# Kernel tuning notes

Measured on AMD Instinct MI355X. Metric: run time of the kernel, lower is better.

Reference implementation:

```python
import jax, jax.numpy as jnp
import numpy as np

P = 2        # patch size
NH = 16      # num heads
HD = 64      # head dim
OC = 4       # out channels
EPS_RMS = 1e-6
EPS_LN = 1e-5

def rmsnorm(x, w):
    return x * jax.lax.rsqrt(jnp.mean(x * x, -1, keepdims=True) + EPS_RMS) * w

def layernorm(x):  # elementwise_affine=False
    m = jnp.mean(x, -1, keepdims=True)
    v = jnp.mean((x - m) ** 2, -1, keepdims=True)
    return (x - m) * jax.lax.rsqrt(v + EPS_LN)

def rope_cache(n, hd):
    inv = 1.0 / (10000.0 ** (jnp.arange(0, hd, 2, dtype=jnp.float32) / hd))
    fr = jnp.arange(n, dtype=jnp.float32)[:, None] * inv[None, :]
    emb = jnp.concatenate([fr, fr], -1)  # [N, hd]
    return jnp.cos(emb), jnp.sin(emb)

def rotate_half(x):
    x1, x2 = jnp.split(x, 2, -1)
    return jnp.concatenate([-x2, x1], -1)

def setup_inputs() -> dict:
    key = jax.random.key(0)
    ks = iter(jax.random.split(key, 48))
    B, D, C, Sw = 8, 4, 1024, 2730
    def w(shape, s=0.02):
        return jax.random.normal(next(ks), shape, jnp.float32) * s
    return dict(
        x=jax.random.normal(next(ks), (B, 4, 32, 32), jnp.float32),
        y=jax.random.randint(next(ks), (B,), 0, 1000),
        cfg_scale=jax.random.uniform(next(ks), (B,), jnp.float32),
        patch_w=w((C, 16)), patch_b=jnp.zeros((C,), jnp.float32),
        pos_embed=w((1, 256, C)),
        class_embed=w((1001, C)),
        cfg_w1=w((C, 1)), cfg_b1=jnp.zeros((C,), jnp.float32),
        cfg_w2=w((C, C)), cfg_b2=jnp.zeros((C,), jnp.float32),
        blk_norm1_w=jnp.ones((D, C), jnp.float32), blk_norm2_w=jnp.ones((D, C), jnp.float32),
        blk_qkv_w=w((D, 3 * C, C)),
        blk_proj_w=w((D, C, C)), blk_proj_b=jnp.zeros((D, C), jnp.float32),
        blk_qn_w=jnp.ones((D, HD), jnp.float32), blk_kn_w=jnp.ones((D, HD), jnp.float32),
        blk_w1=w((D, Sw, C)), blk_w2=w((D, C, Sw)), blk_w3=w((D, Sw, C)),
        blk_ada_w=w((D, 6 * C, C)), blk_ada_b=jnp.zeros((D, 6 * C), jnp.float32),
        fin_ada_w=w((2 * C, C)), fin_ada_b=jnp.zeros((2 * C,), jnp.float32),
        fin_lin_w=w((P * P * OC, C)), fin_lin_b=jnp.zeros((P * P * OC,), jnp.float32),
    )

def reference(x, y, cfg_scale, patch_w, patch_b, pos_embed, class_embed,
              cfg_w1, cfg_b1, cfg_w2, cfg_b2,
              blk_norm1_w, blk_norm2_w, blk_qkv_w, blk_proj_w, blk_proj_b,
              blk_qn_w, blk_kn_w, blk_w1, blk_w2, blk_w3, blk_ada_w, blk_ada_b,
              fin_ada_w, fin_ada_b, fin_lin_w, fin_lin_b):
    B, Ci, Hi, Wi = x.shape
    h = Hi // P
    N = h * h
    C = patch_w.shape[0]
    scale = HD ** -0.5

    # patch embed: conv(k=2,s=2) == per-patch matmul with (Ci,p,p)-flattened weight
    patches = x.reshape(B, Ci, h, P, h, P).transpose(0, 2, 4, 1, 3, 5).reshape(B, N, Ci * P * P)
    tok = patches @ patch_w.T + patch_b + pos_embed  # [B,N,C]

    # conditioning: class embedding + cfg-scale MLP
    c = class_embed[y]
    hc = jax.nn.silu(cfg_scale[:, None] @ cfg_w1.T + cfg_b1)
    c = c + hc @ cfg_w2.T + cfg_b2  # [B,C]
    silu_c = jax.nn.silu(c)

    cos, sin = rope_cache(N, HD)  # [N,HD]
    cos = cos[None, None]
    sin = sin[None, None]

    def block(xc, p):
        n1w, n2w, qkvw, projw, projb, qnw, knw, w1, w2, w3, adaw, adab = p
        mods = silu_c @ adaw.T + adab  # [B,6C]
        sm, scm, gm, smlp, sclp, glp = jnp.split(mods, 6, -1)
        # attention branch
        xm = rmsnorm(xc, n1w) * (1 + scm[:, None]) + sm[:, None]
        qkv = (xm @ qkvw.T).reshape(B, N, 3, NH, HD).transpose(2, 0, 3, 1, 4)
        q, k, v = qkv[0], qkv[1], qkv[2]  # [B,NH,N,HD]
        q = rmsnorm(q, qnw)
        k = rmsnorm(k, knw)
        q = q * cos + rotate_half(q) * sin
        k = k * cos + rotate_half(k) * sin
        attn = jax.nn.softmax(jnp.einsum('bhqd,bhkd->bhqk', q, k) * scale, axis=-1)
        o = jnp.einsum('bhqk,bhkd->bhqd', attn, v).transpose(0, 2, 1, 3).reshape(B, N, C)
        xc = xc + gm[:, None] * (o @ projw.T + projb)
        # SwiGLU MLP branch
        xm = rmsnorm(xc, n2w) * (1 + sclp[:, None]) + smlp[:, None]
        mlp = (jax.nn.silu(xm @ w1.T) * (xm @ w3.T)) @ w2.T
        xc = xc + glp[:, None] * mlp
        return xc, None

    blk_params = (blk_norm1_w, blk_norm2_w, blk_qkv_w, blk_proj_w, blk_proj_b,
                  blk_qn_w, blk_kn_w, blk_w1, blk_w2, blk_w3, blk_ada_w, blk_ada_b)
    tok, _ = jax.lax.scan(block, tok, blk_params)

    # final layer
    shift, scl = jnp.split(silu_c @ fin_ada_w.T + fin_ada_b, 2, -1)
    out = layernorm(tok) * (1 + scl[:, None]) + shift[:, None]
    out = out @ fin_lin_w.T + fin_lin_b  # [B,N,P*P*OC]

    # unpatchify: (B,h,w,p,p,c) -> (B,c,h*p,w*p)
    out = out.reshape(B, h, h, P, P, OC).transpose(0, 5, 1, 3, 2, 4).reshape(B, OC, h * P, h * P)
    return out
```

## Files before the change

### kernel.cpp

```cpp
#include <hip/hip_runtime.h>

typedef unsigned char u8;
typedef unsigned short u16;
typedef unsigned int u32;
typedef float f32x4 __attribute__((ext_vector_type(4)));
typedef __bf16 bf16x8 __attribute__((ext_vector_type(8)));

#define DEV __device__ __forceinline__

DEV u16 f2bf(float f) {
  u32 u = __builtin_bit_cast(u32, f);
  u += 0x7fffu + ((u >> 16) & 1u);
  return (u16)(u >> 16);
}
DEV float bf2f(u16 u) { return __builtin_bit_cast(float, (u32)u << 16); }
DEV u32 f2f8(float f) {
  u32 u = __builtin_bit_cast(u32, f);
  u32 s = (u >> 31) << 7;
  float a = __builtin_fabsf(f);
  if (a >= 448.f) return s | 0x7Eu;
  if (a < 0.015625f) {
    int m = (int)(a * 512.f + 0.5f);
    return s | (u32)m;
  }
  u32 b = __builtin_bit_cast(u32, a);
  b += 0x7FFFFu + ((b >> 20) & 1u);
  u32 E = (b >> 23) - 120u;
  if (E > 15u) return s | 0x7Eu;
  return s | (E << 3) | ((b >> 20) & 7u);
}
DEV u32 pk4f8(float x, float y, float z, float w) {
  return f2f8(x) | (f2f8(y) << 8) | (f2f8(z) << 16) | (f2f8(w) << 24);
}
DEV float waveAllSum(float x) {
#pragma unroll
  for (int off = 32; off > 0; off >>= 1) x += __shfl_xor(x, off, 64);
  return x;
}
DEV float silu_f(float x) { return x / (1.f + __expf(-x)); }

DEV void gll16(const void* g, void* l) {
  __builtin_amdgcn_global_load_lds(
      (const __attribute__((address_space(1))) void*)g,
      (__attribute__((address_space(3))) void*)l, 16, 0, 0);
}

template<int BM, int BN, int EPI>
__global__ __launch_bounds__(256, (BM == 128 ? 2 : 3)) void gemm8_t(
    const u8* __restrict__ A, int lda,
    const u8* __restrict__ W, int ldw,
    int Ksteps, int nbx,
    float* __restrict__ RX, const float* __restrict__ gmods,
    const float* __restrict__ bias,
    u16* __restrict__ ob0, u16* __restrict__ ob1, u16* __restrict__ ob2,
    u8* __restrict__ h1o,
    const float* __restrict__ nw_q, const float* __restrict__ nw_k)
{
  constexpr int MI = BM / 32;
  constexpr int NJ = BN / 32;
  constexpr int LOADS = (BM + BN) / 32;
  __shared__ long As[2][BM][16];
  __shared__ long Ws[2][BN][16];
  const int tid = threadIdx.x;
  const int lane = tid & 63;
  const int wave = tid >> 6;
  const int nwg = gridDim.x;
  const int cpx = nwg >> 3;
  const int fb = blockIdx.x;
  const int idx = (fb & 7) * cpx + (fb >> 3);
  const int m0 = (idx % nbx) * BM;
  const int n0 = (idx / nbx) * BN;
  const int wm = (wave >> 1) * (BM / 2);
  const int wn = (wave & 1) * (BN / 2);
  const int rl = lane & 15;
  const int qq = lane >> 4;
  const u8* Abase = A + (size_t)m0 * lda;
  const u8* Wbase = W + (size_t)n0 * ldw;

  f32x4 acc[MI][NJ];
#pragma unroll
  for (int i = 0; i < MI; ++i)
#pragma unroll
    for (int j = 0; j < NJ; ++j) acc[i][j] = (f32x4){0.f, 0.f, 0.f, 0.f};

  auto STAGE = [&](int buf, int k0) {
#pragma unroll
    for (int c = 0; c < BM / 32; ++c) {
      const int flat = c * 256 + tid;
      const int row = flat >> 3;
      const int ch = flat & 7;
      gll16(Abase + (size_t)row * lda + k0 + ((ch ^ (row & 7)) << 4),
            &As[buf][row][ch * 2]);
    }
#pragma unroll
    for (int c = 0; c < BN / 32; ++c) {
      const int flat = c * 256 + tid;
      const int row = flat >> 3;
      const int ch = flat & 7;
      gll16(Wbase + (size_t)row * ldw + k0 + ((ch ^ (row & 7)) << 4),
            &Ws[buf][row][ch * 2]);
    }
  };

  STAGE(0, 0);
  for (int kt = 0; kt < Ksteps; ++kt) {
    const int buf = kt & 1;
    if (kt + 1 < Ksteps) {
      STAGE(buf ^ 1, (kt + 1) * 128);
      if constexpr (LOADS == 8)
        asm volatile("s_waitcnt vmcnt(8)" ::: "memory");
      else if constexpr (LOADS == 6)
        asm volatile("s_waitcnt vmcnt(6)" ::: "memory");
      else
        asm volatile("s_waitcnt vmcnt(4)" ::: "memory");
    } else {
      asm volatile("s_waitcnt vmcnt(0)" ::: "memory");
    }
    __builtin_amdgcn_s_barrier();
    __builtin_amdgcn_sched_barrier(0);
#pragma unroll
    for (int kk = 0; kk < 4; ++kk) {
      const int lo = (((kk * 2 + (qq >> 1)) ^ (rl & 7)) << 1) | (qq & 1);
      long af[MI];
#pragma unroll
      for (int i = 0; i < MI; ++i) af[i] = As[buf][wm + i * 16 + rl][lo];
      long bw[NJ];
#pragma unroll
      for (int j = 0; j < NJ; ++j) bw[j] = Ws[buf][wn + j * 16 + rl][lo];
#pragma unroll
      for (int i = 0; i < MI; ++i)
#pragma unroll
        for (int j = 0; j < NJ; ++j)
          acc[i][j] = __builtin_amdgcn_mfma_f32_16x16x32_fp8_fp8(af[i], bw[j], acc[i][j], 0, 0, 0);
    }
    __builtin_amdgcn_sched_barrier(0);
    __builtin_amdgcn_s_barrier();
  }

  constexpr float S = 0.0625f;
  const int rq = qq * 4;
  if constexpr (EPI == 1) {
    const int b = m0 >> 8;
    const float* gm = gmods + (size_t)b * 6144;
#pragma unroll
    for (int j = 0; j < NJ; ++j) {
      const int n = n0 + wn + j * 16 + rl;
      const float g = gm[n];
      const float bv = bias ? bias[n] : 0.f;
#pragma unroll
      for (int i = 0; i < MI; ++i) {
        const int mrow = m0 + wm + i * 16 + rq;
#pragma unroll
        for (int r = 0; r < 4; ++r) {
          float* p = RX + (size_t)(mrow + r) * 1024 + n;
          *p += g * (acc[i][j][r] * S + bv);
        }
      }
    }
  } else if constexpr (EPI == 2) {
    const int region = n0 >> 10;
    const int h = ((n0 + wn) >> 6) & 15;
    const int bh = (m0 >> 8) * 16 + h;
    if (region == 2) {
#pragma unroll
      for (int i = 0; i < MI; ++i)
#pragma unroll
        for (int r = 0; r < 4; ++r) {
          const int token = (m0 + wm + i * 16 + rq + r) & 255;
          u16* dst = ob2 + ((size_t)bh * 256 + token) * 64 + rl;
#pragma unroll
          for (int j = 0; j < 4; ++j) dst[j * 16] = f2bf(acc[i][j][r] * S);
        }
    } else {
      const float* nw = region ? nw_k : nw_q;
      u16* obuf = region ? ob1 : ob0;
      float wv[4];
#pragma unroll
      for (int j = 0; j < 4; ++j) wv[j] = nw[j * 16 + rl];
      const float f0 = __powf(10000.f, -(float)(2 * rl) * (1.f / 64.f));
      const float f1 = __powf(10000.f, -(float)(2 * (16 + rl)) * (1.f / 64.f));
#pragma unroll
      for (int i = 0; i < MI; ++i) {
        float va[4][4];
        float ss[4];
#pragma unroll
        for (int r = 0; r < 4; ++r) {
          ss[r] = 0.f;
#pragma unroll
          for (int j = 0; j < 4; ++j) {
            va[j][r] = acc[i][j][r] * S;
            ss[r] += va[j][r] * va[j][r];
          }
        }
#pragma unroll
        for (int off = 1; off < 16; off <<= 1)
#pragma unroll
          for (int r = 0; r < 4; ++r) ss[r] += __shfl_xor(ss[r], off, 64);
#pragma unroll
        for (int r = 0; r < 4; ++r) {
          const int token = (m0 + wm + i * 16 + rq + r) & 255;
          const float rms = rsqrtf(ss[r] * (1.f / 64.f) + 1e-6f);
          float nv[4];
#pragma unroll
          for (int j = 0; j < 4; ++j) nv[j] = va[j][r] * rms * wv[j];
          float s0, c0, s1, c1;
          __sincosf((float)token * f0, &s0, &c0);
          __sincosf((float)token * f1, &s1, &c1);
          u16* dst = obuf + ((size_t)bh * 256 + token) * 64 + rl;
          dst[0]  = f2bf(nv[0] * c0 - nv[2] * s0);
          dst[16] = f2bf(nv[1] * c1 - nv[3] * s1);
          dst[32] = f2bf(nv[2] * c0 + nv[0] * s0);
          dst[48] = f2bf(nv[3] * c1 + nv[1] * s1);
        }
      }
    }
  } else if constexpr (EPI == 3) {
    const int ubase = ((n0 + wn) >> 1) + rl;
#pragma unroll
    for (int i = 0; i < MI; ++i)
#pragma unroll
      for (int r = 0; r < 4; ++r) {
        const int row = m0 + wm + i * 16 + rq + r;
        u8* dst = h1o + (size_t)row * 2816 + ubase;
#pragma unroll
        for (int p = 0; p < 2; ++p) {
          const float a = acc[i][2 * p][r] * S;
          const float b3 = acc[i][2 * p + 1][r] * S;
          dst[p * 16] = (u8)f2f8(silu_f(a) * b3);
        }
      }
  }
}

__global__ __launch_bounds__(256) void conv_qp8_kernel(
    const float* __restrict__ qkvw, const float* __restrict__ projw,
    u8* __restrict__ WB)
{
  for (int g = blockIdx.x * 256 + threadIdx.x; g < 4194304; g += gridDim.x * 256) {
    const int e4 = g * 4;
    const float* src;
    u8* dst;
    if (e4 < 12582912) {
      const int d = e4 / 3145728, off = e4 % 3145728;
      src = qkvw + e4;
      dst = WB + (size_t)d * 12713984 + off;
    } else {
      const int rel = e4 - 12582912;
      const int d = rel / 1048576, off = rel % 1048576;
      src = projw + rel;
      dst = WB + (size_t)d * 12713984 + 3145728 + off;
    }
    float4 v = *(const float4*)src;
    *(u32*)dst = pk4f8(v.x * 16.f, v.y * 16.f, v.z * 16.f, v.w * 16.f);
  }
}

__global__ __launch_bounds__(256) void conv_w138_kernel(
    const float* __restrict__ w1, const float* __restrict__ w3,
    u8* __restrict__ WB)
{
  const int base = blockIdx.x * 4 + (threadIdx.x >> 6);
  const int d = base / 5504, rW = base % 5504;
  const int t = rW >> 5, s = rW & 31;
  const int unit = 16 * t + (s & 15);
  const int lane = threadIdx.x & 63;
  u8* dst = WB + (size_t)d * 12713984 + 4194304 + (size_t)rW * 1024;
  if (unit < 2730) {
    const float* src = ((s < 16) ? w1 : w3) + (size_t)d * 2795520 + (size_t)unit * 1024;
#pragma unroll
    for (int rep = 0; rep < 4; ++rep) {
      float4 v = *(const float4*)(src + rep * 256 + lane * 4);
      *(u32*)(dst + rep * 256 + lane * 4) = pk4f8(v.x * 16.f, v.y * 16.f, v.z * 16.f, v.w * 16.f);
    }
  } else {
#pragma unroll
    for (int rep = 0; rep < 4; ++rep)
      *(u32*)(dst + rep * 256 + lane * 4) = 0;
  }
}

__global__ __launch_bounds__(256) void conv_w28_kernel(
    const float* __restrict__ w2, u8* __restrict__ WB)
{
  const int d = blockIdx.x >> 10, r = blockIdx.x & 1023;
  const float* src = w2 + (size_t)d * 2795520 + (size_t)r * 2730;
  u8* dst = WB + (size_t)d * 12713984 + 9830400 + (size_t)r * 2816;
  for (int c = threadIdx.x * 4; c < 2816; c += 1024) {
    float v[4];
#pragma unroll
    for (int i = 0; i < 4; ++i)
      v[i] = (c + i < 2730) ? src[c + i] * 16.f : 0.f;
    *(u32*)(dst + c) = pk4f8(v[0], v[1], v[2], v[3]);
  }
}

__global__ __launch_bounds__(256) void zt_kernel(u8* __restrict__ h1) {
  const int idx = blockIdx.x * 256 + threadIdx.x;
  const int row = idx >> 4, c = idx & 15;
  *(u32*)(h1 + (size_t)row * 2816 + 2752 + c * 4) = 0;
}

__global__ __launch_bounds__(64) void cond_kernel(
    const float* __restrict__ cfg_s, const float* __restrict__ w1,
    const float* __restrict__ b1, const float* __restrict__ w2,
    const float* __restrict__ b2, const float* __restrict__ ce,
    const int* __restrict__ y, float* __restrict__ sc)
{
  const int j = blockIdx.x, b = blockIdx.y, lane = threadIdx.x;
  const float s = cfg_s[b];
  const float4* wr = (const float4*)(w2 + (size_t)j * 1024);
  const float4* w1r = (const float4*)w1;
  const float4* b1r = (const float4*)b1;
  float acc = 0.f;
#pragma unroll
  for (int rep = 0; rep < 4; ++rep) {
    const int c = rep * 64 + lane;
    float4 w = wr[c];
    float4 a = w1r[c];
    float4 bb = b1r[c];
    acc += w.x * silu_f(s * a.x + bb.x) + w.y * silu_f(s * a.y + bb.y) +
           w.z * silu_f(s * a.z + bb.z) + w.w * silu_f(s * a.w + bb.w);
  }
  acc = waveAllSum(acc);
  if (lane == 0) {
    float v = ce[(size_t)y[b] * 1024 + j] + acc + b2[j];
    sc[(size_t)b * 1024 + j] = silu_f(v);
  }
}

__global__ __launch_bounds__(256, 2) void modlin_ada_kernel(
    const float* __restrict__ adaw, const float* __restrict__ adab,
    const float* __restrict__ finw, const float* __restrict__ finb,
    const float* __restrict__ sc, float* __restrict__ mods,
    float* __restrict__ fmods)
{
  const int tid = threadIdx.x;
  const int lane = tid & 63;
  const int wave = tid >> 6;
  const int j0 = blockIdx.x * 16 + wave * 4;
  float4 sreg[4][8];
#pragma unroll
  for (int rep = 0; rep < 4; ++rep)
#pragma unroll
    for (int b = 0; b < 8; ++b)
      sreg[rep][b] = *(const float4*)(sc + (size_t)b * 1024 + rep * 256 + lane * 4);
  const bool fin = j0 >= 24576;
  const int jrel = fin ? (j0 - 24576) : j0;
  const float* Wb = fin ? finw : adaw;
  const float* Bb = fin ? finb : adab;
#pragma unroll
  for (int r = 0; r < 4; ++r) {
    const int j = jrel + r;
    const float4* wr = (const float4*)(Wb + (size_t)j * 1024);
    float acc[8];
#pragma unroll
    for (int b = 0; b < 8; ++b) acc[b] = 0.f;
#pragma unroll
    for (int rep = 0; rep < 4; ++rep) {
      float4 wv = wr[rep * 64 + lane];
#pragma unroll
      for (int b = 0; b < 8; ++b) {
        float4 s4 = sreg[rep][b];
        acc[b] += wv.x * s4.x + wv.y * s4.y + wv.z * s4.z + wv.w * s4.w;
      }
    }
#pragma unroll
    for (int b = 0; b < 8; ++b) acc[b] = waveAllSum(acc[b]);
    if (lane == 0) {
      const float bb = Bb[j];
      if (fin) {
#pragma unroll
        for (int b = 0; b < 8; ++b) fmods[(size_t)b * 2048 + j] = acc[b] + bb;
      } else {
        const int d = j / 6144;
        const int jj = j - d * 6144;
        float* outb = mods + (size_t)d * 49152;
#pragma unroll
        for (int b = 0; b < 8; ++b) outb[(size_t)b * 6144 + jj] = acc[b] + bb;
      }
    }
  }
}

__global__ __launch_bounds__(256) void patch_kernel(
    const float* __restrict__ x, const float* __restrict__ pw,
    const float* __restrict__ pb, const float* __restrict__ pos,
    float* __restrict__ xc)
{
  const int n = blockIdx.x, b = blockIdx.y, tid = threadIdx.x;
  __shared__ float pv[16];
  if (tid < 16) {
    const int ci = tid >> 2, pi = (tid >> 1) & 1, pj = tid & 1;
    const int i = n >> 4, j = n & 15;
    pv[tid] = x[((size_t)(b * 4 + ci) * 32 + i * 2 + pi) * 32 + j * 2 + pj];
  }
  __syncthreads();
#pragma unroll
  for (int qq = 0; qq < 4; ++qq) {
    const int c = qq * 256 + tid;
    const float4* wr = (const float4*)(pw + (size_t)c * 16);
    float acc = pb[c] + pos[(size_t)n * 1024 + c];
#pragma unroll
    for (int g = 0; g < 4; ++g) {
      float4 w = wr[g];
      acc += w.x * pv[g * 4] + w.y * pv[g * 4 + 1] + w.z * pv[g * 4 + 2] + w.w * pv[g * 4 + 3];
    }
    xc[((size_t)b * 256 + n) * 1024 + c] = acc;
  }
}

__global__ __launch_bounds__(256) void normmod8_kernel(
    const float* __restrict__ xc, const float* __restrict__ w,
    const float* __restrict__ mods, int mult_off, int shift_off,
    u8* __restrict__ out)
{
  const int m = blockIdx.x, b = m >> 8, tid = threadIdx.x;
  const float* row = xc + (size_t)m * 1024;
  float4 v = *(const float4*)(row + tid * 4);
  float ss = v.x * v.x + v.y * v.y + v.z * v.z + v.w * v.w;
  ss = waveAllSum(ss);
  __shared__ float red[4];
  if ((tid & 63) == 0) red[tid >> 6] = ss;
  __syncthreads();
  const float tot = red[0] + red[1] + red[2] + red[3];
  const float r = rsqrtf(tot * (1.f / 1024.f) + 1e-6f);
  const float* mb = mods + (size_t)b * 6144;
  const int c = tid * 4;
  float4 wv = *(const float4*)(w + c);
  float4 mu = *(const float4*)(mb + mult_off + c);
  float4 sh = *(const float4*)(mb + shift_off + c);
  u32 p = pk4f8(v.x * r * wv.x * (1.f + mu.x) + sh.x,
                v.y * r * wv.y * (1.f + mu.y) + sh.y,
                v.z * r * wv.z * (1.f + mu.z) + sh.z,
                v.w * r * wv.w * (1.f + mu.w) + sh.w);
  *(u32*)(out + (size_t)m * 1024 + c) = p;
}

__global__ __launch_bounds__(256) void attn_kernel(
    const u16* __restrict__ qb, const u16* __restrict__ kb,
    const u16* __restrict__ vb, u8* __restrict__ o)
{
  __shared__ alignas(16) u16 Kt[128][72];
  __shared__ alignas(16) u16 Vtt[64][136];
  __shared__ alignas(16) u16 Pw[4][16][136];
  const int bh = blockIdx.x;
  const int qbase = blockIdx.y * 64;
  const int tid = threadIdx.x;
  const int lane = tid & 63;
  const int wave = tid >> 6;
  const int rl = lane & 15;
  const int kq = (lane >> 4) * 8;
  const int rowg = (lane >> 4) * 4;

  const int q0 = qbase + wave * 16;
  const u16* qsrc = qb + ((size_t)bh * 256 + q0 + rl) * 64 + kq;
  const bf16x8 a0 = *(const bf16x8*)(qsrc);
  const bf16x8 a1 = *(const bf16x8*)(qsrc + 32);

  float m[4], l[4];
  f32x4 oacc[4];
#pragma unroll
  for (int r = 0; r < 4; ++r) { m[r] = -1e30f; l[r] = 0.f; }
#pragma unroll
  for (int dt = 0; dt < 4; ++dt) oacc[dt] = (f32x4){0.f, 0.f, 0.f, 0.f};

  for (int kt = 0; kt < 2; ++kt) {
    __syncthreads();
#pragma unroll
    for (int c = 0; c < 4; ++c) {
      const int flat = c * 256 + tid;
      const int row = flat >> 3;
      const int col = (flat & 7) * 8;
      uint4 v = *(const uint4*)(kb + ((size_t)bh * 256 + kt * 128 + row) * 64 + col);
      *(uint4*)&Kt[row][col] = v;
    }
    {
      const int tt = tid & 63;
      const int dh = tid >> 6;
      const int r0 = tt * 2;
      const u16* s0 = vb + ((size_t)bh * 256 + kt * 128 + r0) * 64 + dh * 16;
      const u16* s1 = s0 + 64;
#pragma unroll
      for (int g = 0; g < 2; ++g) {
        uint4 A = *(const uint4*)(s0 + g * 8);
        uint4 B = *(const uint4*)(s1 + g * 8);
        const u32 aw[4] = {A.x, A.y, A.z, A.w};
        const u32 bw[4] = {B.x, B.y, B.z, B.w};
#pragma unroll
        for (int q = 0; q < 4; ++q) {
          const int d2 = dh * 16 + g * 8 + q * 2;
          const u32 lo = (aw[q] & 0xffffu) | (bw[q] << 16);
          const u32 hi = (aw[q] >> 16) | (bw[q] & 0xffff0000u);
          *(u32*)&Vtt[d2][r0] = lo;
          *(u32*)&Vtt[d2 + 1][r0] = hi;
        }
      }
    }
    __syncthreads();

    f32x4 sacc[8];
#pragma unroll
    for (int t = 0; t < 8; ++t) sacc[t] = (f32x4){0.f, 0.f, 0.f, 0.f};
#pragma unroll
    for (int t = 0; t < 8; ++t) {
      bf16x8 k0 = *(const bf16x8*)&Kt[t * 16 + rl][kq];
      bf16x8 k1 = *(const bf16x8*)&Kt[t * 16 + rl][32 + kq];
      sacc[t] = __builtin_amdgcn_mfma_f32_16x16x32_bf16(a0, k0, sacc[t], 0, 0, 0);
      sacc[t] = __builtin_amdgcn_mfma_f32_16x16x32_bf16(a1, k1, sacc[t], 0, 0, 0);
    }
    float cmax[4];
#pragma unroll
    for (int r = 0; r < 4; ++r) cmax[r] = sacc[0][r];
#pragma unroll
    for (int t = 1; t < 8; ++t)
#pragma unroll
      for (int r = 0; r < 4; ++r) cmax[r] = fmaxf(cmax[r], sacc[t][r]);
#pragma unroll
    for (int off = 1; off < 16; off <<= 1)
#pragma unroll
      for (int r = 0; r < 4; ++r) cmax[r] = fmaxf(cmax[r], __shfl_xor(cmax[r], off, 64));
#pragma unroll
    for (int r = 0; r < 4; ++r) {
      const float mn = fmaxf(m[r], cmax[r]);
      const float corr = __expf((m[r] - mn) * 0.125f);
      l[r] *= corr;
#pragma unroll
      for (int dt = 0; dt < 4; ++dt) oacc[dt][r] *= corr;
      m[r] = mn;
    }
    float lsum[4] = {0.f, 0.f, 0.f, 0.f};
#pragma unroll
    for (int t = 0; t < 8; ++t)
#pragma unroll
      for (int r = 0; r < 4; ++r) {
        const float p = __expf((sacc[t][r] - m[r]) * 0.125f);
        lsum[r] += p;
        Pw[wave][rowg + r][t * 16 + rl] = f2bf(p);
      }
#pragma unroll
    for (int off = 1; off < 16; off <<= 1)
#pragma unroll
      for (int r = 0; r < 4; ++r) lsum[r] += __shfl_xor(lsum[r], off, 64);
#pragma unroll
    for (int r = 0; r < 4; ++r) l[r] += lsum[r];
#pragma unroll
    for (int ks = 0; ks < 4; ++ks) {
      bf16x8 pa = *(const bf16x8*)&Pw[wave][rl][ks * 32 + kq];
#pragma unroll
      for (int dt = 0; dt < 4; ++dt) {
        bf16x8 vf = *(const bf16x8*)&Vtt[dt * 16 + rl][ks * 32 + kq];
        oacc[dt] = __builtin_amdgcn_mfma_f32_16x16x32_bf16(pa, vf, oacc[dt], 0, 0, 0);
      }
    }
  }
  const int b = bh >> 4, h = bh & 15;
#pragma unroll
  for (int r = 0; r < 4; ++r) {
    const float inv = 1.f / l[r];
    const int qrow = q0 + rowg + r;
    u8* dst = o + (((size_t)b * 256 + qrow) * 16 + h) * 64 + rl;
#pragma unroll
    for (int dt = 0; dt < 4; ++dt)
      dst[dt * 16] = (u8)f2f8(oacc[dt][r] * inv);
  }
}

__global__ __launch_bounds__(256) void lnmod_kernel(
    const float* __restrict__ xc, const float* __restrict__ fmods,
    u16* __restrict__ out)
{
  const int m = blockIdx.x, b = m >> 8, tid = threadIdx.x;
  const float* row = xc + (size_t)m * 1024;
  float4 v = *(const float4*)(row + tid * 4);
  float s1 = v.x + v.y + v.z + v.w;
  float s2 = v.x * v.x + v.y * v.y + v.z * v.z + v.w * v.w;
  s1 = waveAllSum(s1);
  s2 = waveAllSum(s2);
  __shared__ float r1[4], r2[4];
  if ((tid & 63) == 0) { r1[tid >> 6] = s1; r2[tid >> 6] = s2; }
  __syncthreads();
  const float t1 = r1[0] + r1[1] + r1[2] + r1[3];
  const float t2 = r2[0] + r2[1] + r2[2] + r2[3];
  const float mean = t1 * (1.f / 1024.f);
  const float var = t2 * (1.f / 1024.f) - mean * mean;
  const float rr = rsqrtf(var + 1e-5f);
  const float* mb = fmods + (size_t)b * 2048;
  const int c = tid * 4;
  float4 sh = *(const float4*)(mb + c);
  float4 sl = *(const float4*)(mb + 1024 + c);
  union { u16 u[4]; uint2 v2; } pk;
  pk.u[0] = f2bf((v.x - mean) * rr * (1.f + sl.x) + sh.x);
  pk.u[1] = f2bf((v.y - mean) * rr * (1.f + sl.y) + sh.y);
  pk.u[2] = f2bf((v.z - mean) * rr * (1.f + sl.z) + sh.z);
  pk.u[3] = f2bf((v.w - mean) * rr * (1.f + sl.w) + sh.w);
  *(uint2*)(out + (size_t)m * 1024 + c) = pk.v2;
}

__global__ __launch_bounds__(256) void final_kernel(
    const u16* __restrict__ xfin, const float* __restrict__ w,
    const float* __restrict__ bias, float* __restrict__ out)
{
  const int tid = threadIdx.x;
  const int m = blockIdx.x * 16 + (tid >> 4);
  const int j = tid & 15;
  const u16* xr = xfin + (size_t)m * 1024;
  const float* wr = w + (size_t)j * 1024;
  float acc = 0.f;
  for (int k = 0; k < 1024; k += 8) {
    uint4 xv = *(const uint4*)(xr + k);
    const u16* xu = (const u16*)&xv;
    float4 w0 = *(const float4*)(wr + k);
    float4 w1 = *(const float4*)(wr + k + 4);
    acc += bf2f(xu[0]) * w0.x + bf2f(xu[1]) * w0.y + bf2f(xu[2]) * w0.z + bf2f(xu[3]) * w0.w;
    acc += bf2f(xu[4]) * w1.x + bf2f(xu[5]) * w1.y + bf2f(xu[6]) * w1.z + bf2f(xu[7]) * w1.w;
  }
  acc += bias[j];
  const int b = m >> 8, n = m & 255;
  const int i = n >> 4, jj = n & 15;
  const int pi = (j >> 3) & 1, pj = (j >> 2) & 1, oc = j & 3;
  out[((size_t)(b * 4 + oc) * 32 + i * 2 + pi) * 32 + jj * 2 + pj] = acc;
}

extern "C" void kernel_launch(void* const* d_in, const int* in_sizes, int n_in,
                              void* d_out, int out_size, void* d_ws, size_t ws_size,
                              hipStream_t stream) {
  const float* x       = (const float*)d_in[0];
  const int*   y       = (const int*)  d_in[1];
  const float* cfg_s   = (const float*)d_in[2];
  const float* patch_w = (const float*)d_in[3];
  const float* patch_b = (const float*)d_in[4];
  const float* pos_e   = (const float*)d_in[5];
  const float* class_e = (const float*)d_in[6];
  const float* cfg_w1  = (const float*)d_in[7];
  const float* cfg_b1  = (const float*)d_in[8];
  const float* cfg_w2  = (const float*)d_in[9];
  const float* cfg_b2  = (const float*)d_in[10];
  const float* n1w     = (const float*)d_in[11];
  const float* n2w     = (const float*)d_in[12];
  const float* qkvw    = (const float*)d_in[13];
  const float* projw   = (const float*)d_in[14];
  const float* projb   = (const float*)d_in[15];
  const float* qnw     = (const float*)d_in[16];
  const float* knw     = (const float*)d_in[17];
  const float* w1      = (const float*)d_in[18];
  const float* w2      = (const float*)d_in[19];
  const float* w3      = (const float*)d_in[20];
  const float* adaw    = (const float*)d_in[21];
  const float* adab    = (const float*)d_in[22];
  const float* finaw   = (const float*)d_in[23];
  const float* finab   = (const float*)d_in[24];
  const float* flw     = (const float*)d_in[25];
  const float* flb     = (const float*)d_in[26];
  (void)in_sizes; (void)n_in; (void)out_size;

  char* ws = (char*)d_ws;
  const size_t MB = 1024 * 1024;
  if (ws_size < 96 * MB) return;
  float* sc    = (float*)(ws + 32 * 1024);
  float* mods  = (float*)(ws + 64 * 1024);
  float* fmods = (float*)(ws + 64 * 1024 + 786432);
  float* xc    = (float*)(ws + 1 * MB);
  u8*    xm8   = (u8*)   (ws + 9 * MB);
  u16*   qbuf  = (u16*)  (ws + 11 * MB);
  u16*   kbuf  = (u16*)  (ws + 15 * MB);
  u16*   vbuf  = (u16*)  (ws + 19 * MB);
  u8*    h18   = (u8*)   (ws + 23 * MB);
  u16*   lnbuf = (u16*)  (ws + 29 * MB);
  u8*    WB    = (u8*)   (ws + 33 * MB);
  const size_t LSTR = 12713984;

  cond_kernel<<<dim3(1024, 8), 64, 0, stream>>>(cfg_s, cfg_w1, cfg_b1, cfg_w2,
                                                cfg_b2, class_e, y, sc);
  modlin_ada_kernel<<<1664, 256, 0, stream>>>(adaw, adab, finaw, finab, sc,
                                              mods, fmods);
  patch_kernel<<<dim3(256, 8), 256, 0, stream>>>(x, patch_w, patch_b, pos_e, xc);
  conv_qp8_kernel<<<8192, 256, 0, stream>>>(qkvw, projw, WB);
  conv_w138_kernel<<<5504, 256, 0, stream>>>(w1, w3, WB);
  conv_w28_kernel<<<4096, 256, 0, stream>>>(w2, WB);
  zt_kernel<<<128, 256, 0, stream>>>(h18);

  for (int d = 0; d < 4; ++d) {
    const float* md = mods + (size_t)d * 49152;
    u8* WL = WB + (size_t)d * LSTR;
    normmod8_kernel<<<2048, 256, 0, stream>>>(xc, n1w + d * 1024, md, 1024, 0, xm8);
    gemm8_t<64, 128, 2><<<768, 256, 0, stream>>>(xm8, 1024, WL, 1024, 8, 32,
                                                 nullptr, nullptr, nullptr,
                                                 qbuf, kbuf, vbuf, nullptr,
                                                 qnw + d * 64, knw + d * 64);
    attn_kernel<<<dim3(128, 4), 256, 0, stream>>>(qbuf, kbuf, vbuf, xm8);
    gemm8_t<64, 64, 1><<<512, 256, 0, stream>>>(xm8, 1024, WL + 3145728, 1024, 8, 32,
                                                xc, md + 2048, projb + d * 1024,
                                                nullptr, nullptr, nullptr, nullptr,
                                                nullptr, nullptr);
    normmod8_kernel<<<2048, 256, 0, stream>>>(xc, n2w + d * 1024, md, 4096, 3072, xm8);
    gemm8_t<128, 128, 3><<<688, 256, 0, stream>>>(xm8, 1024, WL + 4194304, 1024, 8, 16,
                                                  nullptr, nullptr, nullptr,
                                                  nullptr, nullptr, nullptr, h18,
                                                  nullptr, nullptr);
    gemm8_t<64, 64, 1><<<512, 256, 0, stream>>>(h18, 2816, WL + 9830400, 2816, 22, 32,
                                                xc, md + 5120, nullptr,
                                                nullptr, nullptr, nullptr, nullptr,
                                                nullptr, nullptr);
  }

  lnmod_kernel<<<2048, 256, 0, stream>>>(xc, fmods, lnbuf);
  final_kernel<<<128, 256, 0, stream>>>(lnbuf, flw, flb, (float*)d_out);
}
```

Baseline: 605.4 us.

## Merge weight-conversion kernels, fuse final layernorm with projection, retile W13 GEMM

Folds the three weight-conversion kernels into one launch using block-range dispatch, and fuses the final layernorm-modulate into the final projection through a shared-memory bf16 staging tile, which removes one launch and the lnbuf round trip. The SwiGLU W1/W3 GEMM moves from 128x128 to 64x128 tiles with twice the blocks. Launch bounds for 64x64 tiles rise to 4 waves per SIMD. The fused final kernel runs only 128 blocks, so its layernorm phase has less parallelism than the old 2048-block kernel.

```diff
diff --git a/kernel.cpp b/kernel.cpp
--- a/kernel.cpp
+++ b/kernel.cpp
@@ -46,7 +46,8 @@
 }
 
 template<int BM, int BN, int EPI>
-__global__ __launch_bounds__(256, (BM == 128 ? 2 : 3)) void gemm8_t(
+__global__ __launch_bounds__(256, (BM == 128 ? 2 : ((BM + BN) == 128 ? 4 : 3)))
+void gemm8_t(
     const u8* __restrict__ A, int lda,
     const u8* __restrict__ W, int ldw,
     int Ksteps, int nbx,
@@ -232,65 +233,61 @@
   }
 }
 
-__global__ __launch_bounds__(256) void conv_qp8_kernel(
+__global__ __launch_bounds__(256) void conv_all_kernel(
     const float* __restrict__ qkvw, const float* __restrict__ projw,
-    u8* __restrict__ WB)
-{
-  for (int g = blockIdx.x * 256 + threadIdx.x; g < 4194304; g += gridDim.x * 256) {
-    const int e4 = g * 4;
-    const float* src;
-    u8* dst;
-    if (e4 < 12582912) {
-      const int d = e4 / 3145728, off = e4 % 3145728;
-      src = qkvw + e4;
-      dst = WB + (size_t)d * 12713984 + off;
-    } else {
-      const int rel = e4 - 12582912;
-      const int d = rel / 1048576, off = rel % 1048576;
-      src = projw + rel;
-      dst = WB + (size_t)d * 12713984 + 3145728 + off;
-    }
-    float4 v = *(const float4*)src;
-    *(u32*)dst = pk4f8(v.x * 16.f, v.y * 16.f, v.z * 16.f, v.w * 16.f);
-  }
-}
-
-__global__ __launch_bounds__(256) void conv_w138_kernel(
     const float* __restrict__ w1, const float* __restrict__ w3,
-    u8* __restrict__ WB)
-{
-  const int base = blockIdx.x * 4 + (threadIdx.x >> 6);
-  const int d = base / 5504, rW = base % 5504;
-  const int t = rW >> 5, s = rW & 31;
-  const int unit = 16 * t + (s & 15);
-  const int lane = threadIdx.x & 63;
-  u8* dst = WB + (size_t)d * 12713984 + 4194304 + (size_t)rW * 1024;
-  if (unit < 2730) {
-    const float* src = ((s < 16) ? w1 : w3) + (size_t)d * 2795520 + (size_t)unit * 1024;
-#pragma unroll
-    for (int rep = 0; rep < 4; ++rep) {
-      float4 v = *(const float4*)(src + rep * 256 + lane * 4);
-      *(u32*)(dst + rep * 256 + lane * 4) = pk4f8(v.x * 16.f, v.y * 16.f, v.z * 16.f, v.w * 16.f);
-    }
-  } else {
-#pragma unroll
-    for (int rep = 0; rep < 4; ++rep)
-      *(u32*)(dst + rep * 256 + lane * 4) = 0;
-  }
-}
-
-__global__ __launch_bounds__(256) void conv_w28_kernel(
     const float* __restrict__ w2, u8* __restrict__ WB)
 {
-  const int d = blockIdx.x >> 10, r = blockIdx.x & 1023;
-  const float* src = w2 + (size_t)d * 2795520 + (size_t)r * 2730;
-  u8* dst = WB + (size_t)d * 12713984 + 9830400 + (size_t)r * 2816;
-  for (int c = threadIdx.x * 4; c < 2816; c += 1024) {
-    float v[4];
-#pragma unroll
-    for (int i = 0; i < 4; ++i)
-      v[i] = (c + i < 2730) ? src[c + i] * 16.f : 0.f;
-    *(u32*)(dst + c) = pk4f8(v[0], v[1], v[2], v[3]);
+  const int bid = blockIdx.x;
+  if (bid < 8192) {
+    for (int g = bid * 256 + threadIdx.x; g < 4194304; g += 8192 * 256) {
+      const int e4 = g * 4;
+      const float* src;
+      u8* dst;
+      if (e4 < 12582912) {
+        const int d = e4 / 3145728, off = e4 % 3145728;
+        src = qkvw + e4;
+        dst = WB + (size_t)d * 12713984 + off;
+      } else {
+        const int rel = e4 - 12582912;
+        const int d = rel / 1048576, off = rel % 1048576;
+        src = projw + rel;
+        dst = WB + (size_t)d * 12713984 + 3145728 + off;
+      }
+      float4 v = *(const float4*)src;
+      *(u32*)dst = pk4f8(v.x * 16.f, v.y * 16.f, v.z * 16.f, v.w * 16.f);
+    }
+  } else if (bid < 13696) {
+    const int base = (bid - 8192) * 4 + (threadIdx.x >> 6);
+    const int d = base / 5504, rW = base % 5504;
+    const int t = rW >> 5, s = rW & 31;
+    const int unit = 16 * t + (s & 15);
+    const int lane = threadIdx.x & 63;
+    u8* dst = WB + (size_t)d * 12713984 + 4194304 + (size_t)rW * 1024;
+    if (unit < 2730) {
+      const float* src = ((s < 16) ? w1 : w3) + (size_t)d * 2795520 + (size_t)unit * 1024;
+#pragma unroll
+      for (int rep = 0; rep < 4; ++rep) {
+        float4 v = *(const float4*)(src + rep * 256 + lane * 4);
+        *(u32*)(dst + rep * 256 + lane * 4) = pk4f8(v.x * 16.f, v.y * 16.f, v.z * 16.f, v.w * 16.f);
+      }
+    } else {
+#pragma unroll
+      for (int rep = 0; rep < 4; ++rep)
+        *(u32*)(dst + rep * 256 + lane * 4) = 0;
+    }
+  } else {
+    const int rc = bid - 13696;
+    const int d = rc >> 10, r = rc & 1023;
+    const float* src = w2 + (size_t)d * 2795520 + (size_t)r * 2730;
+    u8* dst = WB + (size_t)d * 12713984 + 9830400 + (size_t)r * 2816;
+    for (int c = threadIdx.x * 4; c < 2816; c += 1024) {
+      float v[4];
+#pragma unroll
+      for (int i = 0; i < 4; ++i)
+        v[i] = (c + i < 2730) ? src[c + i] * 16.f : 0.f;
+      *(u32*)(dst + c) = pk4f8(v[0], v[1], v[2], v[3]);
+    }
   }
 }
 
@@ -565,49 +562,57 @@
   }
 }
 
-__global__ __launch_bounds__(256) void lnmod_kernel(
+__global__ __launch_bounds__(256) void lnfinal_kernel(
     const float* __restrict__ xc, const float* __restrict__ fmods,
-    u16* __restrict__ out)
+    const float* __restrict__ w, const float* __restrict__ bias,
+    float* __restrict__ out)
 {
-  const int m = blockIdx.x, b = m >> 8, tid = threadIdx.x;
-  const float* row = xc + (size_t)m * 1024;
-  float4 v = *(const float4*)(row + tid * 4);
-  float s1 = v.x + v.y + v.z + v.w;
-  float s2 = v.x * v.x + v.y * v.y + v.z * v.z + v.w * v.w;
-  s1 = waveAllSum(s1);
-  s2 = waveAllSum(s2);
-  __shared__ float r1[4], r2[4];
-  if ((tid & 63) == 0) { r1[tid >> 6] = s1; r2[tid >> 6] = s2; }
+  __shared__ alignas(16) u16 xb[16][1024];
+  const int tid = threadIdx.x;
+  const int lane = tid & 63;
+  const int wave = tid >> 6;
+  const int mbase = blockIdx.x * 16;
+#pragma unroll
+  for (int rr = 0; rr < 4; ++rr) {
+    const int mloc = wave * 4 + rr;
+    const int m = mbase + mloc;
+    const int b = m >> 8;
+    const float* row = xc + (size_t)m * 1024;
+    float4 v[4];
+    float s1 = 0.f, s2 = 0.f;
+#pragma unroll
+    for (int g = 0; g < 4; ++g) {
+      v[g] = *(const float4*)(row + g * 256 + lane * 4);
+      s1 += v[g].x + v[g].y + v[g].z + v[g].w;
+      s2 += v[g].x * v[g].x + v[g].y * v[g].y + v[g].z * v[g].z + v[g].w * v[g].w;
+    }
+    s1 = waveAllSum(s1);
+    s2 = waveAllSum(s2);
+    const float mean = s1 * (1.f / 1024.f);
+    const float var = s2 * (1.f / 1024.f) - mean * mean;
+    const float rstd = rsqrtf(var + 1e-5f);
+    const float* mb = fmods + (size_t)b * 2048;
+#pragma unroll
+    for (int g = 0; g < 4; ++g) {
+      const int c = g * 256 + lane * 4;
+      float4 sh = *(const float4*)(mb + c);
+      float4 sl = *(const float4*)(mb + 1024 + c);
+      union { u16 u[4]; uint2 v2; } pk;
+      pk.u[0] = f2bf((v[g].x - mean) * rstd * (1.f + sl.x) + sh.x);
+      pk.u[1] = f2bf((v[g].y - mean) * rstd * (1.f + sl.y) + sh.y);
+      pk.u[2] = f2bf((v[g].z - mean) * rstd * (1.f + sl.z) + sh.z);
+      pk.u[3] = f2bf((v[g].w - mean) * rstd * (1.f + sl.w) + sh.w);
+      *(uint2*)&xb[mloc][c] = pk.v2;
+    }
+  }
   __syncthreads();
-  const float t1 = r1[0] + r1[1] + r1[2] + r1[3];
-  const float t2 = r2[0] + r2[1] + r2[2] + r2[3];
-  const float mean = t1 * (1.f / 1024.f);
-  const float var = t2 * (1.f / 1024.f) - mean * mean;
-  const float rr = rsqrtf(var + 1e-5f);
-  const float* mb = fmods + (size_t)b * 2048;
-  const int c = tid * 4;
-  float4 sh = *(const float4*)(mb + c);
-  float4 sl = *(const float4*)(mb + 1024 + c);
-  union { u16 u[4]; uint2 v2; } pk;
-  pk.u[0] = f2bf((v.x - mean) * rr * (1.f + sl.x) + sh.x);
-  pk.u[1] = f2bf((v.y - mean) * rr * (1.f + sl.y) + sh.y);
-  pk.u[2] = f2bf((v.z - mean) * rr * (1.f + sl.z) + sh.z);
-  pk.u[3] = f2bf((v.w - mean) * rr * (1.f + sl.w) + sh.w);
-  *(uint2*)(out + (size_t)m * 1024 + c) = pk.v2;
-}
-
-__global__ __launch_bounds__(256) void final_kernel(
-    const u16* __restrict__ xfin, const float* __restrict__ w,
-    const float* __restrict__ bias, float* __restrict__ out)
-{
-  const int tid = threadIdx.x;
-  const int m = blockIdx.x * 16 + (tid >> 4);
+  const int mloc = tid >> 4;
   const int j = tid & 15;
-  const u16* xr = xfin + (size_t)m * 1024;
+  const int m = mbase + mloc;
   const float* wr = w + (size_t)j * 1024;
   float acc = 0.f;
   for (int k = 0; k < 1024; k += 8) {
-    uint4 xv = *(const uint4*)(xr + k);
+    uint4 xv = *(const uint4*)&xb[mloc][k];
     const u16* xu = (const u16*)&xv;
     float4 w0 = *(const float4*)(wr + k);
     float4 w1 = *(const float4*)(wr + k + 4);
@@ -665,7 +670,6 @@
   u16*   kbuf  = (u16*)  (ws + 15 * MB);
   u16*   vbuf  = (u16*)  (ws + 19 * MB);
   u8*    h18   = (u8*)   (ws + 23 * MB);
-  u16*   lnbuf = (u16*)  (ws + 29 * MB);
   u8*    WB    = (u8*)   (ws + 33 * MB);
   const size_t LSTR = 12713984;
 
@@ -674,9 +678,7 @@
   modlin_ada_kernel<<<1664, 256, 0, stream>>>(adaw, adab, finaw, finab, sc,
                                               mods, fmods);
   patch_kernel<<<dim3(256, 8), 256, 0, stream>>>(x, patch_w, patch_b, pos_e, xc);
-  conv_qp8_kernel<<<8192, 256, 0, stream>>>(qkvw, projw, WB);
-  conv_w138_kernel<<<5504, 256, 0, stream>>>(w1, w3, WB);
-  conv_w28_kernel<<<4096, 256, 0, stream>>>(w2, WB);
+  conv_all_kernel<<<17792, 256, 0, stream>>>(qkvw, projw, w1, w3, w2, WB);
   zt_kernel<<<128, 256, 0, stream>>>(h18);
 
   for (int d = 0; d < 4; ++d) {
@@ -693,7 +695,7 @@
                                                 nullptr, nullptr, nullptr, nullptr,
                                                 nullptr, nullptr);
     normmod8_kernel<<<2048, 256, 0, stream>>>(xc, n2w + d * 1024, md, 4096, 3072, xm8);
-    gemm8_t<128, 128, 3><<<688, 256, 0, stream>>>(xm8, 1024, WL + 4194304, 1024, 8, 16,
+    gemm8_t<64, 128, 3><<<1376, 256, 0, stream>>>(xm8, 1024, WL + 4194304, 1024, 8, 32,
                                                   nullptr, nullptr, nullptr,
                                                   nullptr, nullptr, nullptr, h18,
                                                   nullptr, nullptr);
@@ -703,6 +705,5 @@
                                                 nullptr, nullptr);
   }
 
-  lnmod_kernel<<<2048, 256, 0, stream>>>(xc, fmods, lnbuf);
-  final_kernel<<<128, 256, 0, stream>>>(lnbuf, flw, flb, (float*)d_out);
-}
+  lnfinal_kernel<<<128, 256, 0, stream>>>(xc, fmods, flw, flb, (float*)d_out);
+}
```

Result: faster. 565.3 us (-6.6%).
